# Optimization experiments

Measured on AMD Instinct MI355X. Metric: run time of the kernel, lower is better.

Reference implementation:

```python
import jax, jax.numpy as jnp
import numpy as np

BLOCK = 9      # photometric_loss block size
LOSS_EPS = 0.5 # census ternary threshold


def _sign_eps(d, eps):
    # ternary census: -1 / 0 / +1 with dead-zone eps
    return jnp.where(d < -eps, -1.0, jnp.where(d > eps, 1.0, 0.0))


def _census_sad(es, ta, block, eps):
    # per-pixel mean over valid 9x9 window of |census(es) - census(ta)|
    B, C, H, W = es.shape
    P = block // 2
    pad = ((0, 0), (0, 0), (P, P), (P, P))
    esp = jnp.pad(es, pad)
    tap = jnp.pad(ta, pad)
    vp = jnp.pad(jnp.ones((1, 1, H, W), es.dtype), pad)  # validity of shifted px
    total = jnp.zeros_like(es)
    count = jnp.zeros((1, 1, H, W), es.dtype)
    for dh in range(-P, P + 1):          # fixed 9x9 structural loop
        for dw in range(-P, P + 1):
            es_s = esp[:, :, P + dh:P + dh + H, P + dw:P + dw + W]
            ta_s = tap[:, :, P + dh:P + dh + H, P + dw:P + dw + W]
            v = vp[:, :, P + dh:P + dh + H, P + dw:P + dw + W]
            c = jnp.abs(_sign_eps(es_s - es, eps) - _sign_eps(ta_s - ta, eps))
            total = total + v * c
            count = count + v
    return total / count


def reference(disp0, im, pattern):
    B, _, H, W = disp0.shape
    # pattern.mean(dim=1, keepdim=True)
    pat = jnp.broadcast_to(pattern.mean(axis=1, keepdims=True), (B, 1, H, W))
    # grid_sample(align_corners=True, border) with y unchanged reduces to
    # clamped 1D linear interpolation along width at x = u - disp
    u = jnp.arange(W, dtype=disp0.dtype)
    x = jnp.clip(u[None, None, None, :] - disp0, 0.0, W - 1)  # [B,1,H,W]
    x0 = jnp.floor(x).astype(jnp.int32)
    x1 = jnp.minimum(x0 + 1, W - 1)
    w = x - x0.astype(x.dtype)
    p0 = jnp.take_along_axis(pat, x0, axis=3)
    p1 = jnp.take_along_axis(pat, x1, axis=3)
    pattern_proj = p0 * (1.0 - w) + p1 * w
    diff = _census_sad(pattern_proj, im, BLOCK, LOSS_EPS)
    # mask = ones (std=None): (mask*diff).sum()/mask.sum() == mean
    val = diff.mean()
    return val, pattern_proj


def setup_inputs() -> dict:
    key = jax.random.key(0)
    k1, k2, k3 = jax.random.split(key, 3)
    B, H, W = 16, 512, 640
    disp0 = jax.random.uniform(k1, (B, 1, H, W), dtype=jnp.float32) * 64.0
    im = jax.random.uniform(k2, (B, 1, H, W), dtype=jnp.float32)
    pattern = jax.random.uniform(k3, (1, 3, H, W), dtype=jnp.float32)
    return {"disp0": disp0, "im": im, "pattern": pattern}
```

## Files before the change

kernel.cpp:

```cpp
#include <hip/hip_runtime.h>

#define BB 16
#define HH 512
#define WW 640
constexpr int HW = HH * WW;

#define WT 64
#define HT 32
#define PAD 4
#define LW (WT + 2*PAD)
#define LH (HT + PAD)
#define GX (WW / WT)
#define GY (HH / HT)
#define NBLK (GX * GY * BB)

typedef _Float16 h2 __attribute__((ext_vector_type(2)));

constexpr float HALO = 30000.0f;

__device__ __forceinline__ float fast_rcp(float x) {
#if __has_builtin(__builtin_amdgcn_rcpf)
    return __builtin_amdgcn_rcpf(x);
#else
    return 1.0f / x;
#endif
}

__device__ __forceinline__ _Float16 habs(_Float16 x) {
    union { _Float16 h; unsigned short u; } v;
    v.h = x; v.u &= 0x7fffu;
    return v.h;
}

template<bool EDGE>
__device__ __forceinline__ float census_sum(const h2* sm, int tx, int rg,
                                            int bx, int by)
{
    const h2 K2   = { (_Float16)1536.0f, (_Float16)1536.0f };
    const h2 ONE2 = { (_Float16)1.0f,  (_Float16)1.0f };
    const h2 NEG2 = { (_Float16)-1.0f, (_Float16)-1.0f };

    float invcw[9];
    if constexpr (EDGE) {
        int w0 = bx * WT + tx;
        #pragma unroll
        for (int j = 0; j < 9; ++j) {
            int c  = w0 + j - 4;
            int cw = min(4, WW - 1 - c) + min(4, c) + 1;
            invcw[j] = fast_rcp((float)cw);
        }
    }

    float tsum = 0.0f;
    #pragma unroll 1
    for (int p = 0; p < 8; ++p) {
        const int lr = rg * 8 + p;
        const h2* base = sm + lr * LW + tx;
        const h2 ct = base[PAD];

        float invch[5], wp;
        float facc = 0.0f;
        _Float16 hacc = (_Float16)0.0f;
        if constexpr (EDGE) {
            int r0 = by * HT + lr;
            #pragma unroll
            for (int d = 0; d < 5; ++d) {
                int r  = r0 + d;
                int ch = min(4, HH - 1 - r) + min(4, r) + 1;
                invch[d] = fast_rcp((float)ch);
            }
            wp = invch[0] * invcw[4];
        }

        auto tap = [&](int dh, int j) {
            h2 d2 = base[dh * LW + j] - ct;
            d2 = __builtin_elementwise_max(d2, NEG2);
            d2 = __builtin_elementwise_min(d2, ONE2);
            d2 = d2 + K2;
            d2 = d2 - K2;
            _Float16 diff = d2.x - d2.y;
            if constexpr (EDGE) {
                float c  = fabsf((float)diff);
                float wt = fmaf(invch[dh], invcw[j], wp);
                facc = fmaf(c, wt, facc);
            } else {
                hacc = hacc + habs(diff);
            }
        };

        #pragma unroll
        for (int j = 5; j <= 8; ++j) tap(0, j);
        #pragma unroll
        for (int dh = 1; dh <= 4; ++dh) {
            #pragma unroll
            for (int j = 0; j <= 8; ++j) tap(dh, j);
        }

        tsum += EDGE ? facc : (float)hacc;
    }
    return tsum;
}

__global__ __launch_bounds__(256)
void fused_kernel(const float* __restrict__ disp0,
                  const float* __restrict__ im,
                  const float* __restrict__ pattern,
                  float* __restrict__ out,
                  float* __restrict__ partial)
{
    __shared__ h2 sm[LH * LW];
    __shared__ float wsum[4];

    const int bx = blockIdx.x, by = blockIdx.y, b = blockIdx.z;
    const int tx = threadIdx.x;
    const int rg = threadIdx.y;
    const int tid = rg * 64 + tx;

    const float* db = disp0 + (size_t)b * HW;
    const float* ib = im    + (size_t)b * HW;
    float* proj = out + 1 + (size_t)b * HW;

    const int gh0 = by * HT;
    const int gw0 = bx * WT - PAD;

    #pragma unroll
    for (int it = 0; it < (LH * LW + 255) / 256; ++it) {
        int i = tid + it * 256;
        if (i < LH * LW) {
            int lh = i / LW;
            int lw = i - lh * LW;
            int gh = gh0 + lh, gw = gw0 + lw;
            float ev = HALO, tv = HALO;
            if ((gh < HH) & (gw >= 0) & (gw < WW)) {
                int g = gh * WW + gw;
                float d = db[g];
                float x = fminf(fmaxf((float)gw - d, 0.0f), (float)(WW - 1));
                int   x0 = (int)x;
                int   x1 = min(x0 + 1, WW - 1);
                float w  = x - (float)x0;
                const float* prow = pattern + gh * WW;
                float p0 = (prow[x0] + prow[HW + x0] + prow[2*HW + x0]) * (1.0f/3.0f);
                float p1 = (prow[x1] + prow[HW + x1] + prow[2*HW + x1]) * (1.0f/3.0f);
                ev = p0 * (1.0f - w) + p1 * w;
                tv = ib[g];
                if ((lh < HT) & (lw >= PAD) & (lw < PAD + WT))
                    proj[g] = ev;
            }
            h2 pk = { (_Float16)ev, (_Float16)tv };
            sm[i] = pk;
        }
    }
    __syncthreads();

    float tsum;
    if ((bx >= 1) & (bx <= GX - 2) & (by >= 1) & (by <= GY - 2)) {
        tsum = census_sum<false>(sm, tx, rg, bx, by) * (2.0f / 81.0f);
    } else {
        tsum = census_sum<true>(sm, tx, rg, bx, by);
    }

    #pragma unroll
    for (int off = 32; off > 0; off >>= 1)
        tsum += __shfl_down(tsum, off, 64);
    if (tx == 0) wsum[rg] = tsum;
    __syncthreads();
    if (tid == 0)
        partial[(b * GY + by) * GX + bx] = wsum[0] + wsum[1] + wsum[2] + wsum[3];
}

__global__ __launch_bounds__(256)
void reduce_kernel(const float* __restrict__ partial, float* __restrict__ out)
{
    __shared__ float wsum[4];
    int t = threadIdx.x;
    float s = 0.0f;
    #pragma unroll
    for (int i = 0; i < NBLK / 256; ++i) s += partial[t + i * 256];
    #pragma unroll
    for (int off = 32; off > 0; off >>= 1)
        s += __shfl_down(s, off, 64);
    if ((t & 63) == 0) wsum[t >> 6] = s;
    __syncthreads();
    if (t == 0)
        out[0] = (wsum[0] + wsum[1] + wsum[2] + wsum[3]) * (1.0f / ((float)BB * (float)HW));
}

extern "C" void kernel_launch(void* const* d_in, const int* in_sizes, int n_in,
                              void* d_out, int out_size, void* d_ws, size_t ws_size,
                              hipStream_t stream) {
    const float* disp0   = (const float*)d_in[0];
    const float* im      = (const float*)d_in[1];
    const float* pattern = (const float*)d_in[2];
    float* out = (float*)d_out;
    float* partial = (float*)d_ws;

    dim3 grid(GX, GY, BB);
    dim3 block(64, 4);
    fused_kernel<<<grid, block, 0, stream>>>(disp0, im, pattern, out, partial);
    reduce_kernel<<<1, 256, 0, stream>>>(partial, out);
}
```

Measured before the change: 158.9 us.

## Rewrite census as threshold-compare counts with register row reuse and fp32 tiles

The interior census no longer computes a ternary sign difference in packed fp16. It counts mismatches between paired threshold comparisons (x > c+eps and x < c-eps) as integers, which gives the same absolute difference. Each thread now handles 4 output rows and loads each window row once from LDS into registers, reusing it across those rows. The tile height drops from 32 to 16 and LDS holds separate fp32 arrays for es and ta. The aim is fewer LDS reads per tap and cheaper compare-based arithmetic, at the cost of more blocks, a larger halo fraction and more register pressure.

New measurement: 171.2 us. 1.08x slower.

```diff
diff --git a/kernel.cpp b/kernel.cpp
--- a/kernel.cpp
+++ b/kernel.cpp
@@ -6,7 +6,8 @@
 constexpr int HW = HH * WW;
 
 #define WT 64
-#define HT 32
+#define HT 16
+#define RP 4
 #define PAD 4
 #define LW (WT + 2*PAD)
 #define LH (HT + PAD)
@@ -14,91 +15,115 @@
 #define GY (HH / HT)
 #define NBLK (GX * GY * BB)
 
-typedef _Float16 h2 __attribute__((ext_vector_type(2)));
-
-constexpr float HALO = 30000.0f;
+constexpr float HALO = 1.0e6f;
 
 __device__ __forceinline__ float fast_rcp(float x) {
-#if __has_builtin(__builtin_amdgcn_rcpf)
     return __builtin_amdgcn_rcpf(x);
-#else
-    return 1.0f / x;
-#endif
-}
-
-__device__ __forceinline__ _Float16 habs(_Float16 x) {
-    union { _Float16 h; unsigned short u; } v;
-    v.h = x; v.u &= 0x7fffu;
-    return v.h;
-}
-
-template<bool EDGE>
-__device__ __forceinline__ float census_sum(const h2* sm, int tx, int rg,
-                                            int bx, int by)
-{
-    const h2 K2   = { (_Float16)1536.0f, (_Float16)1536.0f };
-    const h2 ONE2 = { (_Float16)1.0f,  (_Float16)1.0f };
-    const h2 NEG2 = { (_Float16)-1.0f, (_Float16)-1.0f };
-
+}
+
+__device__ __forceinline__ float census_interior(const float* es_t, const float* ta_t,
+                                                 int tx, int rg)
+{
+    float ehi[RP], elo[RP], thi[RP], tlo[RP];
+    #pragma unroll
+    for (int p = 0; p < RP; ++p) {
+        int lr = rg * RP + p;
+        float ec = es_t[lr * LW + tx + PAD];
+        float tc = ta_t[lr * LW + tx + PAD];
+        ehi[p] = ec + 0.5f;  elo[p] = ec - 0.5f;
+        thi[p] = tc + 0.5f;  tlo[p] = tc - 0.5f;
+    }
+
+    int acca[RP] = {0, 0, 0, 0};
+    int accb[RP] = {0, 0, 0, 0};
+
+    #pragma unroll
+    for (int wr = 0; wr < RP + PAD; ++wr) {
+        const int lr = rg * RP + wr;
+        float e[9], t[9];
+        #pragma unroll
+        for (int j = 0; j < 9; ++j) {
+            e[j] = es_t[lr * LW + tx + j];
+            t[j] = ta_t[lr * LW + tx + j];
+        }
+        if (wr < RP) {
+            #pragma unroll
+            for (int j = 5; j <= 8; ++j) {
+                acca[wr] += (int)((e[j] > ehi[wr]) != (t[j] > thi[wr]));
+                accb[wr] += (int)((e[j] < elo[wr]) != (t[j] < tlo[wr]));
+            }
+        }
+        #pragma unroll
+        for (int p = 0; p < RP; ++p) {
+            if (p <= wr - 1 && p >= wr - PAD) {
+                #pragma unroll
+                for (int j = 0; j <= 8; ++j) {
+                    acca[p] += (int)((e[j] > ehi[p]) != (t[j] > thi[p]));
+                    accb[p] += (int)((e[j] < elo[p]) != (t[j] < tlo[p]));
+                }
+            }
+        }
+    }
+    int acc = (acca[0] + acca[1]) + (acca[2] + acca[3])
+            + (accb[0] + accb[1]) + (accb[2] + accb[3]);
+    return (float)acc;
+}
+
+__device__ __forceinline__ float census_edge(const float* es_t, const float* ta_t,
+                                             int tx, int rg, int bx, int by)
+{
     float invcw[9];
-    if constexpr (EDGE) {
-        int w0 = bx * WT + tx;
+    const int w0 = bx * WT + tx;
+    #pragma unroll
+    for (int j = 0; j < 9; ++j) {
+        int c  = w0 + j - PAD;
+        int cw = min(PAD, WW - 1 - c) + min(PAD, c) + 1;
+        invcw[j] = fast_rcp((float)cw);
+    }
+    float rowinv[RP + PAD];
+    #pragma unroll
+    for (int wr = 0; wr < RP + PAD; ++wr) {
+        int r  = by * HT + rg * RP + wr;
+        int ch = min(PAD, HH - 1 - r) + min(PAD, r) + 1;
+        rowinv[wr] = fast_rcp((float)ch);
+    }
+
+    float ec[RP], tc[RP], wp[RP], facc[RP];
+    #pragma unroll
+    for (int p = 0; p < RP; ++p) {
+        int lr = rg * RP + p;
+        ec[p] = es_t[lr * LW + tx + PAD];
+        tc[p] = ta_t[lr * LW + tx + PAD];
+        wp[p] = rowinv[p] * invcw[PAD];
+        facc[p] = 0.0f;
+    }
+
+    #pragma unroll
+    for (int wr = 0; wr < RP + PAD; ++wr) {
+        const int lr = rg * RP + wr;
+        float e[9], t[9];
         #pragma unroll
         for (int j = 0; j < 9; ++j) {
-            int c  = w0 + j - 4;
-            int cw = min(4, WW - 1 - c) + min(4, c) + 1;
-            invcw[j] = fast_rcp((float)cw);
-        }
-    }
-
-    float tsum = 0.0f;
-    #pragma unroll 1
-    for (int p = 0; p < 8; ++p) {
-        const int lr = rg * 8 + p;
-        const h2* base = sm + lr * LW + tx;
-        const h2 ct = base[PAD];
-
-        float invch[5], wp;
-        float facc = 0.0f;
-        _Float16 hacc = (_Float16)0.0f;
-        if constexpr (EDGE) {
-            int r0 = by * HT + lr;
-            #pragma unroll
-            for (int d = 0; d < 5; ++d) {
-                int r  = r0 + d;
-                int ch = min(4, HH - 1 - r) + min(4, r) + 1;
-                invch[d] = fast_rcp((float)ch);
-            }
-            wp = invch[0] * invcw[4];
-        }
-
-        auto tap = [&](int dh, int j) {
-            h2 d2 = base[dh * LW + j] - ct;
-            d2 = __builtin_elementwise_max(d2, NEG2);
-            d2 = __builtin_elementwise_min(d2, ONE2);
-            d2 = d2 + K2;
-            d2 = d2 - K2;
-            _Float16 diff = d2.x - d2.y;
-            if constexpr (EDGE) {
-                float c  = fabsf((float)diff);
-                float wt = fmaf(invch[dh], invcw[j], wp);
-                facc = fmaf(c, wt, facc);
-            } else {
-                hacc = hacc + habs(diff);
-            }
-        };
-
-        #pragma unroll
-        for (int j = 5; j <= 8; ++j) tap(0, j);
-        #pragma unroll
-        for (int dh = 1; dh <= 4; ++dh) {
-            #pragma unroll
-            for (int j = 0; j <= 8; ++j) tap(dh, j);
-        }
-
-        tsum += EDGE ? facc : (float)hacc;
-    }
-    return tsum;
+            e[j] = es_t[lr * LW + tx + j];
+            t[j] = ta_t[lr * LW + tx + j];
+        }
+        #pragma unroll
+        for (int p = 0; p < RP; ++p) {
+            const bool d0 = (p == wr);
+            if (p <= wr && p >= wr - PAD) {
+                #pragma unroll
+                for (int j = 0; j <= 8; ++j) {
+                    if (d0 && j <= 4) continue;
+                    float s1 = rintf(__builtin_amdgcn_fmed3f(e[j] - ec[p], -1.0f, 1.0f));
+                    float s2 = rintf(__builtin_amdgcn_fmed3f(t[j] - tc[p], -1.0f, 1.0f));
+                    float c  = fabsf(s1 - s2);
+                    float wt = fmaf(rowinv[wr], invcw[j], wp[p]);
+                    facc[p] = fmaf(c, wt, facc[p]);
+                }
+            }
+        }
+    }
+    return (facc[0] + facc[1]) + (facc[2] + facc[3]);
 }
 
 __global__ __launch_bounds__(256)
@@ -108,7 +133,8 @@
                   float* __restrict__ out,
                   float* __restrict__ partial)
 {
-    __shared__ h2 sm[LH * LW];
+    __shared__ float es_t[LH * LW];
+    __shared__ float ta_t[LH * LW];
     __shared__ float wsum[4];
 
     const int bx = blockIdx.x, by = blockIdx.y, b = blockIdx.z;
@@ -146,17 +172,17 @@
                 if ((lh < HT) & (lw >= PAD) & (lw < PAD + WT))
                     proj[g] = ev;
             }
-            h2 pk = { (_Float16)ev, (_Float16)tv };
-            sm[i] = pk;
+            es_t[i] = ev;
+            ta_t[i] = tv;
         }
     }
     __syncthreads();
 
     float tsum;
     if ((bx >= 1) & (bx <= GX - 2) & (by >= 1) & (by <= GY - 2)) {
-        tsum = census_sum<false>(sm, tx, rg, bx, by) * (2.0f / 81.0f);
+        tsum = census_interior(es_t, ta_t, tx, rg) * (2.0f / 81.0f);
     } else {
-        tsum = census_sum<true>(sm, tx, rg, bx, by);
+        tsum = census_edge(es_t, ta_t, tx, rg, bx, by);
     }
 
     #pragma unroll
```
